# Kernel tuning notes

Measured on AMD Instinct MI355X. Metric: run time of the kernel, lower is better.

The kernel has to match this reference:

```python
import jax, jax.numpy as jnp
import numpy as np

B = 16; H = 64; WRES = 64; C = 512; NH = 16; WH = 8; WW = 8; PATCH = 4
N = WH * WW; HD = C // NH; R_MAX = PATCH * H; HID = 4 * C
PI = 3.141592653589793


def _rel_coords():
    yy, xx = np.meshgrid(np.arange(WH), np.arange(WW), indexing='ij')
    flat = np.stack([yy.ravel(), xx.ravel()])  # (2, N)
    rel = flat[:, :, None] - flat[:, None, :]  # (2, N, N)
    return rel[0].astype(np.int32), rel[1].astype(np.int32)

RAD_NP, AZ_NP = _rel_coords()


def _ln(x, g, b):
    m = x.mean(-1, keepdims=True)
    v = ((x - m) ** 2).mean(-1, keepdims=True)
    return (x - m) / jnp.sqrt(v + 1e-5) * g + b


def setup_inputs() -> dict:
    key = jax.random.key(0)
    ks = jax.random.split(key, 12)
    s = 0.02
    return {
        'x': jax.random.normal(ks[0], (B, H * WRES, C), jnp.float32),
        'D': jax.random.uniform(ks[1], (B, H, WRES), jnp.float32),
        'norm1_g': jnp.ones((C,), jnp.float32), 'norm1_b': jnp.zeros((C,), jnp.float32),
        'qkv_w': jax.random.normal(ks[2], (3 * C, C), jnp.float32) * s,
        'qkv_b': jnp.zeros((3 * C,), jnp.float32),
        'proj_w': jax.random.normal(ks[3], (C, C), jnp.float32) * s,
        'proj_b': jnp.zeros((C,), jnp.float32),
        'a_p': jax.random.normal(ks[4], (2 * WW - 1, NH), jnp.float32) * s,
        'b_p': jax.random.normal(ks[5], (2 * WW - 1, NH), jnp.float32) * s,
        'a_r': jax.random.normal(ks[6], (2 * WH - 1, NH), jnp.float32) * s,
        'b_r': jax.random.normal(ks[7], (2 * WH - 1, NH), jnp.float32) * s,
        'norm2_g': jnp.ones((C,), jnp.float32), 'norm2_b': jnp.zeros((C,), jnp.float32),
        'fc1_w': jax.random.normal(ks[8], (HID, C), jnp.float32) * s,
        'fc1_b': jnp.zeros((HID,), jnp.float32),
        'fc2_w': jax.random.normal(ks[9], (C, HID), jnp.float32) * s,
        'fc2_b': jnp.zeros((C,), jnp.float32),
    }


def reference(x, D, norm1_g, norm1_b, qkv_w, qkv_b, proj_w, proj_b,
              a_p, b_p, a_r, b_r, norm2_g, norm2_b, fc1_w, fc1_b, fc2_w, fc2_b):
    rad = jnp.asarray(RAD_NP)  # (N, N) relative row offsets in [-(WH-1), WH-1]
    az = jnp.asarray(AZ_NP)    # (N, N) relative col offsets
    shortcut = x
    xn = _ln(x, norm1_g, norm1_b).reshape(B, H, WRES, C)
    # window partition: (B,H,W,C) -> (nW*B, N, C); same for D -> (nW*B, N)
    xw = xn.reshape(B, H // WH, WH, WRES // WW, WW, C).transpose(0, 1, 3, 2, 4, 5).reshape(-1, N, C)
    Dw = D.reshape(B, H // WH, WH, WRES // WW, WW).transpose(0, 1, 3, 2, 4).reshape(-1, N)
    # qkv: (B_, N, 3C) -> q,k,v (B_, NH, N, HD)
    qkv = (xw @ qkv_w.T + qkv_b).reshape(-1, N, 3, NH, HD).transpose(2, 0, 3, 1, 4)
    q, k, v = qkv[0], qkv[1], qkv[2]
    q = q * (HD ** -0.5)
    attn = jnp.einsum('bhnd,bhmd->bhnm', q, k)
    # A_phi: gathered azimuth tables + trig, (N, N, NH). torch negative index == idx % size
    ip = az % (2 * WW - 1)
    azf = az.astype(jnp.float32) * (2.0 * PI / WRES)
    A_phi = a_p[ip] * jnp.cos(azf)[..., None] + b_p[ip] * jnp.sin(azf)[..., None]
    # A_r: per-window depth-modulated radius, (B_, N, N, NH); rad_final[b,i,j] = rad[i,j]*D[b,j]
    ir = rad % (2 * WH - 1)
    ang = (rad.astype(jnp.float32)[None] * Dw[:, None, :]) * (2.0 * PI / R_MAX)
    A_r = a_r[ir][None] * jnp.cos(ang)[..., None] + b_r[ir][None] * jnp.sin(ang)[..., None]
    attn = attn + jnp.transpose(A_phi, (2, 0, 1))[None] + jnp.transpose(A_r, (0, 3, 1, 2))
    attn = jax.nn.softmax(attn, axis=-1)
    out = jnp.einsum('bhnm,bhmd->bhnd', attn, v).transpose(0, 2, 1, 3).reshape(-1, N, C)
    out = out @ proj_w.T + proj_b
    # window reverse -> (B, H*W, C)
    xr = out.reshape(B, H // WH, WRES // WW, WH, WW, C).transpose(0, 1, 3, 2, 4, 5).reshape(B, H * WRES, C)
    x = shortcut + xr
    xm = _ln(x, norm2_g, norm2_b)
    h = jax.nn.gelu(xm @ fc1_w.T + fc1_b, approximate=False)
    return x + (h @ fc2_w.T + fc2_b)
```

## Files before the change

### kernel.cpp

```cpp
#include <hip/hip_runtime.h>
#include <hip/hip_bf16.h>
#include <math.h>

typedef __hip_bfloat16 bf16;
using f32x4  = __attribute__((ext_vector_type(4))) float;
using bf16x8 = __attribute__((ext_vector_type(8))) short;

static __device__ __forceinline__ float b2f(bf16 v) { return __bfloat162float(v); }
static __device__ __forceinline__ short f2b_s(float f) {
    bf16 b = __float2bfloat16(f);
    return *reinterpret_cast<short*>(&b);
}

static __device__ __forceinline__ void gl_lds16(const void* g, void* l) {
    __builtin_amdgcn_global_load_lds(
        (const __attribute__((address_space(1))) unsigned int*)g,
        (__attribute__((address_space(3))) unsigned int*)l, 16, 0, 0);
}

__global__ __launch_bounds__(256) void f2b_kernel(const float* __restrict__ in,
                                                  short* __restrict__ out, int n4)
{
    int i = blockIdx.x * 256 + threadIdx.x;
    if (i < n4) {
        float4 f = reinterpret_cast<const float4*>(in)[i];
        short4 s;
        s.x = f2b_s(f.x); s.y = f2b_s(f.y); s.z = f2b_s(f.z); s.w = f2b_s(f.w);
        reinterpret_cast<short4*>(out)[i] = s;
    }
}

__global__ __launch_bounds__(64) void ln_kernel(
    const float* __restrict__ in, const float* __restrict__ g,
    const float* __restrict__ bta, bf16* __restrict__ out, int windowed)
{
    int lr  = blockIdx.x;
    int tid = threadIdx.x;
    const float* xr = in + (size_t)lr * 512;
    int c0 = tid * 8;
    float4 f0 = *reinterpret_cast<const float4*>(xr + c0);
    float4 f1 = *reinterpret_cast<const float4*>(xr + c0 + 4);
    float v[8] = { f0.x, f0.y, f0.z, f0.w, f1.x, f1.y, f1.z, f1.w };
    float s = 0.f, s2 = 0.f;
#pragma unroll
    for (int k = 0; k < 8; ++k) { s += v[k]; s2 += v[k] * v[k]; }
#pragma unroll
    for (int off = 32; off; off >>= 1) {
        s  += __shfl_xor(s,  off, 64);
        s2 += __shfl_xor(s2, off, 64);
    }
    float mean = s * (1.0f / 512.0f);
    float var  = s2 * (1.0f / 512.0f) - mean * mean;
    float inv  = rsqrtf(var + 1e-5f);
    size_t drow;
    if (windowed) {
        int b_loc = lr >> 12;
        int l  = lr & 4095;
        int gr = l >> 6, gc = l & 63;
        int wy = gr >> 3, iy = gr & 7, wx = gc >> 3, ix = gc & 7;
        drow = (size_t)((b_loc * 64 + wy * 8 + wx) * 64 + iy * 8 + ix);
    } else {
        drow = (size_t)lr;
    }
    bf16* orow = out + drow * 512;
#pragma unroll
    for (int k = 0; k < 8; ++k) {
        int c = c0 + k;
        orow[c] = __float2bfloat16((v[k] - mean) * inv * g[c] + bta[c]);
    }
}

__global__ __launch_bounds__(256) void gemm_mfma(
    const bf16* __restrict__ A, const short* __restrict__ W,
    const float* __restrict__ bias, int N, int K, int mode,
    void* __restrict__ dstv, const float* __restrict__ res)
{
    __shared__ short As0[128 * 32];
    __shared__ short Bs0[128 * 32];
    __shared__ short As1[128 * 32];
    __shared__ short Bs1[128 * 32];

    int tid  = threadIdx.x;
    int wave = tid >> 6, lane = tid & 63;
    int waveM = wave >> 1, waveN = wave & 1;

    int nx  = gridDim.x;
    int nwg = nx * gridDim.y;
    int lid = blockIdx.y * nx + blockIdx.x;
    int nid = lid;
    if ((nwg & 7) == 0) nid = (lid & 7) * (nwg >> 3) + (lid >> 3);
    int mBase = (nid / nx) * 128;
    int nBase = (nid % nx) * 128;

    f32x4 acc[4][4] = {};

    int rr   = wave * 32 + (lane >> 2);
    int segE = (lane & 3) * 8;
    const bf16*  Ag = A + (size_t)(mBase + rr) * K + segE;
    const short* Bg = W + (size_t)(nBase + rr) * K + segE;
    size_t rs16 = (size_t)16 * K;

    int mf = waveM * 64 + (lane & 15);
    int nf = waveN * 64 + (lane & 15);
    int kq = (lane >> 4) * 8;

    auto stage = [&](int kb, short* Ad, short* Bd) {
        gl_lds16(Ag + kb,        Ad + wave * 1024);
        gl_lds16(Ag + kb + rs16, Ad + wave * 1024 + 512);
        gl_lds16(Bg + kb,        Bd + wave * 1024);
        gl_lds16(Bg + kb + rs16, Bd + wave * 1024 + 512);
    };
    auto compute = [&](const short* As_, const short* Bs_) {
        bf16x8 af[4], bfv[4];
#pragma unroll
        for (int i = 0; i < 4; ++i)
            af[i] = *reinterpret_cast<const bf16x8*>(&As_[(mf + i * 16) * 32 + kq]);
#pragma unroll
        for (int j = 0; j < 4; ++j)
            bfv[j] = *reinterpret_cast<const bf16x8*>(&Bs_[(nf + j * 16) * 32 + kq]);
#pragma unroll
        for (int i = 0; i < 4; ++i)
#pragma unroll
            for (int j = 0; j < 4; ++j)
                acc[i][j] = __builtin_amdgcn_mfma_f32_16x16x32_bf16(af[i], bfv[j], acc[i][j], 0, 0, 0);
    };

    stage(0, As0, Bs0);
    asm volatile("s_waitcnt vmcnt(0)" ::: "memory");
    __builtin_amdgcn_s_barrier();

    int nsteps = K >> 5;
    for (int t = 0; t < nsteps; t += 2) {
        stage((t + 1) << 5, As1, Bs1);
        compute(As0, Bs0);
        asm volatile("s_waitcnt vmcnt(0)" ::: "memory");
        __builtin_amdgcn_s_barrier();
        if (t + 2 < nsteps) stage((t + 2) << 5, As0, Bs0);
        compute(As1, Bs1);
        asm volatile("s_waitcnt vmcnt(0)" ::: "memory");
        __builtin_amdgcn_s_barrier();
    }

    int rq = (lane >> 4) * 4;
#pragma unroll
    for (int j = 0; j < 4; ++j) {
        int n = nBase + waveN * 64 + j * 16 + (lane & 15);
        float bn = bias[n];
#pragma unroll
        for (int i = 0; i < 4; ++i) {
#pragma unroll
            for (int reg = 0; reg < 4; ++reg) {
                int m = mBase + waveM * 64 + i * 16 + rq + reg;
                float v = acc[i][j][reg] + bn;
                if (mode == 0) {
                    ((bf16*)dstv)[(size_t)m * N + n] = __float2bfloat16(v);
                } else if (mode == 1) {
                    int b_loc = m >> 12, w = (m >> 6) & 63, tk = m & 63;
                    int wy = w >> 3, wx = w & 7, iy = tk >> 3, ix = tk & 7;
                    int l = ((wy << 3) + iy) * 64 + (wx << 3) + ix;
                    size_t idx = ((size_t)(b_loc * 4096 + l)) * 512 + n;
                    ((float*)dstv)[idx] = v + res[idx];
                } else if (mode == 2) {
                    float gl = 0.5f * v * (1.0f + erff(v * 0.70710678118654752f));
                    ((bf16*)dstv)[(size_t)m * N + n] = __float2bfloat16(gl);
                } else {
                    size_t idx = (size_t)m * N + n;
                    ((float*)dstv)[idx] = v + res[idx];
                }
            }
        }
    }
}

__global__ __launch_bounds__(256) void attn_kernel(
    const bf16* __restrict__ qkv, const float* __restrict__ Dofs,
    const float* __restrict__ a_p, const float* __restrict__ b_p,
    const float* __restrict__ a_r, const float* __restrict__ b_r,
    bf16* __restrict__ xattn)
{
    __shared__ float cosr[15][64];
    __shared__ float sinr[15][64];
    __shared__ float aphiS[15][16];
    __shared__ float arsS[15][16];
    __shared__ float brsS[15][16];
    __shared__ short Vt[32][72];
    __shared__ short Psh[64][72];

    int b_ = blockIdx.x;
    int bl = b_ >> 6;
    int w  = b_ & 63;
    int wy = w >> 3, wx = w & 7;
    int tid  = threadIdx.x;
    int wave = tid >> 6, lane = tid & 63;

    const float scale = 0.17677669529663687f;
    const float c_az  = 0.09817477042468103f;
    const float c_r   = 0.02454369260617026f;

    for (int t = tid; t < 960; t += 256) {
        int k = t >> 6;
        int j = t & 63;
        int jy = j >> 3, jx = j & 7;
        float Dj  = Dofs[(size_t)bl * 4096 + (wy * 8 + jy) * 64 + (wx * 8 + jx)];
        float ang = (float)(k - 7) * Dj * c_r;
        cosr[k][j] = __cosf(ang);
        sinr[k][j] = __sinf(ang);
    }
    if (tid < 240) {
        int k = tid >> 4;
        int h = tid & 15;
        int v = k - 7;
        int ip = v < 0 ? v + 15 : v;
        float azf = (float)v * c_az;
        aphiS[k][h] = a_p[ip * 16 + h] * __cosf(azf) + b_p[ip * 16 + h] * __sinf(azf);
        arsS[k][h]  = a_r[ip * 16 + h];
        brsS[k][h]  = b_r[ip * 16 + h];
    }

    int i_blk = wave;
    int l15 = lane & 15;
    int lq  = lane >> 4;
    int m0  = i_blk * 16 + lq * 4;
    const bf16* qbase = qkv + (size_t)(b_ * 64) * 1536;
    bf16* obase = xattn + (size_t)(b_ * 64) * 512;

    for (int h = 0; h < 16; ++h) {
        __syncthreads();
        {
            int tok = tid >> 2, dc = (tid & 3) * 8;
            bf16x8 vv = *reinterpret_cast<const bf16x8*>(
                qkv + (size_t)(b_ * 64 + tok) * 1536 + 1024 + h * 32 + dc);
#pragma unroll
            for (int s = 0; s < 8; ++s) Vt[dc + s][tok] = vv[s];
        }
        __syncthreads();

        bf16x8 af = *reinterpret_cast<const bf16x8*>(
            qbase + (size_t)(i_blk * 16 + l15) * 1536 + h * 32 + lq * 8);
        f32x4 Sacc[4] = {};
#pragma unroll
        for (int jb = 0; jb < 4; ++jb) {
            bf16x8 kf = *reinterpret_cast<const bf16x8*>(
                qbase + (size_t)(jb * 16 + l15) * 1536 + 512 + h * 32 + lq * 8);
            Sacc[jb] = __builtin_amdgcn_mfma_f32_16x16x32_bf16(af, kf, Sacc[jb], 0, 0, 0);
        }

        float Sv[4][4];
        float inv[4];
#pragma unroll
        for (int reg = 0; reg < 4; ++reg) {
            int m = m0 + reg;
            int iy = m >> 3, ix = m & 7;
            float rmax = -1e30f;
#pragma unroll
            for (int jb = 0; jb < 4; ++jb) {
                int n = jb * 16 + l15;
                int jy = n >> 3, jx = n & 7;
                int ai = ix - jx + 7;
                int ri = iy - jy + 7;
                float sc = Sacc[jb][reg] * scale + aphiS[ai][h]
                         + arsS[ri][h] * cosr[ri][n] + brsS[ri][h] * sinr[ri][n];
                Sv[reg][jb] = sc;
                rmax = fmaxf(rmax, sc);
            }
#pragma unroll
            for (int off = 1; off <= 8; off <<= 1)
                rmax = fmaxf(rmax, __shfl_xor(rmax, off, 64));
            float rsum = 0.f;
#pragma unroll
            for (int jb = 0; jb < 4; ++jb) {
                float e = __expf(Sv[reg][jb] - rmax);
                Sv[reg][jb] = e;
                rsum += e;
            }
#pragma unroll
            for (int off = 1; off <= 8; off <<= 1)
                rsum += __shfl_xor(rsum, off, 64);
            inv[reg] = 1.0f / rsum;
        }

#pragma unroll
        for (int reg = 0; reg < 4; ++reg)
#pragma unroll
            for (int jb = 0; jb < 4; ++jb)
                Psh[m0 + reg][jb * 16 + l15] = f2b_s(Sv[reg][jb]);

        f32x4 o[2] = {};
#pragma unroll
        for (int ks = 0; ks < 2; ++ks) {
            bf16x8 pa = *reinterpret_cast<const bf16x8*>(
                &Psh[i_blk * 16 + l15][ks * 32 + lq * 8]);
#pragma unroll
            for (int nb = 0; nb < 2; ++nb) {
                bf16x8 bv = *reinterpret_cast<const bf16x8*>(
                    &Vt[nb * 16 + l15][ks * 32 + lq * 8]);
                o[nb] = __builtin_amdgcn_mfma_f32_16x16x32_bf16(pa, bv, o[nb], 0, 0, 0);
            }
        }

#pragma unroll
        for (int nb = 0; nb < 2; ++nb) {
            int d = nb * 16 + l15;
#pragma unroll
            for (int reg = 0; reg < 4; ++reg) {
                int m = m0 + reg;
                obase[(size_t)m * 512 + h * 32 + d] = __float2bfloat16(o[nb][reg] * inv[reg]);
            }
        }
    }
}

extern "C" void kernel_launch(void* const* d_in, const int* in_sizes, int n_in,
                              void* d_out, int out_size, void* d_ws, size_t ws_size,
                              hipStream_t stream)
{
    const float* x      = (const float*)d_in[0];
    const float* D      = (const float*)d_in[1];
    const float* n1g    = (const float*)d_in[2];
    const float* n1b    = (const float*)d_in[3];
    const float* qkv_w  = (const float*)d_in[4];
    const float* qkv_b  = (const float*)d_in[5];
    const float* proj_w = (const float*)d_in[6];
    const float* proj_b = (const float*)d_in[7];
    const float* a_p    = (const float*)d_in[8];
    const float* b_p    = (const float*)d_in[9];
    const float* a_r    = (const float*)d_in[10];
    const float* b_r    = (const float*)d_in[11];
    const float* n2g    = (const float*)d_in[12];
    const float* n2b    = (const float*)d_in[13];
    const float* fc1_w  = (const float*)d_in[14];
    const float* fc1_b  = (const float*)d_in[15];
    const float* fc2_w  = (const float*)d_in[16];
    const float* fc2_b  = (const float*)d_in[17];
    float* out = (float*)d_out;

    char* ws = (char*)d_ws;
    short* qkv_wb  = (short*)ws;
    short* proj_wb = qkv_wb + 786432;
    short* fc1_wb  = proj_wb + 262144;
    short* fc2_wb  = fc1_wb + 1048576;
    char* gws = (char*)(fc2_wb + 1048576);

    int G = 16;
    while (G > 1 && 6291456 + (size_t)G * 4096 * 7168 > ws_size) G >>= 1;
    int NG = 16 / G;
    size_t rowsA = (size_t)G * 4096;

    float* x2   = (float*)gws;
    bf16*  xw   = (bf16*)(gws + rowsA * 2048);
    bf16*  qkvb = xw + rowsA * 512;
    bf16*  xatt = qkvb + rowsA * 1536;
    bf16*  xm   = xw;
    bf16*  hbuf = qkvb;

    hipLaunchKernelGGL(f2b_kernel, dim3(768),  dim3(256), 0, stream, qkv_w,  qkv_wb,  196608);
    hipLaunchKernelGGL(f2b_kernel, dim3(256),  dim3(256), 0, stream, proj_w, proj_wb,  65536);
    hipLaunchKernelGGL(f2b_kernel, dim3(1024), dim3(256), 0, stream, fc1_w,  fc1_wb,  262144);
    hipLaunchKernelGGL(f2b_kernel, dim3(1024), dim3(256), 0, stream, fc2_w,  fc2_wb,  262144);

    int gy = (int)(rowsA / 128);

    for (int g = 0; g < NG; ++g) {
        size_t r0 = (size_t)g * rowsA;
        hipLaunchKernelGGL(ln_kernel, dim3((int)rowsA), dim3(64), 0, stream,
                           x + r0 * 512, n1g, n1b, xw, 1);
        hipLaunchKernelGGL(gemm_mfma, dim3(1536 / 128, gy), dim3(256), 0, stream,
                           xw, qkv_wb, qkv_b, 1536, 512, 0, (void*)qkvb, (const float*)nullptr);
        hipLaunchKernelGGL(attn_kernel, dim3(G * 64), dim3(256), 0, stream,
                           qkvb, D + r0, a_p, b_p, a_r, b_r, xatt);
        hipLaunchKernelGGL(gemm_mfma, dim3(512 / 128, gy), dim3(256), 0, stream,
                           xatt, proj_wb, proj_b, 512, 512, 1, (void*)x2, x + r0 * 512);
        hipLaunchKernelGGL(ln_kernel, dim3((int)rowsA), dim3(64), 0, stream,
                           x2, n2g, n2b, xm, 0);
        hipLaunchKernelGGL(gemm_mfma, dim3(2048 / 128, gy), dim3(256), 0, stream,
                           xm, fc1_wb, fc1_b, 2048, 512, 2, (void*)hbuf, (const float*)nullptr);
        hipLaunchKernelGGL(gemm_mfma, dim3(512 / 128, gy), dim3(256), 0, stream,
                           hbuf, fc2_wb, fc2_b, 512, 2048, 3, (void*)(out + r0 * 512), x2);
    }
}
```

Before: 1.418 ms.

## Triple-buffer GEMM LDS staging with partial vmcnt waits

The GEMM's double-buffered K loop becomes a three-stage LDS ring that prefetches two K-tiles ahead. Each step waits with a partial s_waitcnt vmcnt instead of draining all loads, so global loads overlap more with MFMA compute. This adds 16 KB of LDS per block, which may reduce occupancy, and adds barriers and sched_barriers. The attention grid expression is rewritten but evaluates to the same value.

```diff
diff --git a/kernel.cpp b/kernel.cpp
--- a/kernel.cpp
+++ b/kernel.cpp
@@ -79,6 +79,8 @@
     __shared__ short Bs0[128 * 32];
     __shared__ short As1[128 * 32];
     __shared__ short Bs1[128 * 32];
+    __shared__ short As2[128 * 32];
+    __shared__ short Bs2[128 * 32];
 
     int tid  = threadIdx.x;
     int wave = tid >> 6, lane = tid & 63;
@@ -125,21 +127,33 @@
                 acc[i][j] = __builtin_amdgcn_mfma_f32_16x16x32_bf16(af[i], bfv[j], acc[i][j], 0, 0, 0);
     };
 
-    stage(0, As0, Bs0);
-    asm volatile("s_waitcnt vmcnt(0)" ::: "memory");
-    __builtin_amdgcn_s_barrier();
-
     int nsteps = K >> 5;
-    for (int t = 0; t < nsteps; t += 2) {
-        stage((t + 1) << 5, As1, Bs1);
-        compute(As0, Bs0);
-        asm volatile("s_waitcnt vmcnt(0)" ::: "memory");
-        __builtin_amdgcn_s_barrier();
-        if (t + 2 < nsteps) stage((t + 2) << 5, As0, Bs0);
-        compute(As1, Bs1);
-        asm volatile("s_waitcnt vmcnt(0)" ::: "memory");
-        __builtin_amdgcn_s_barrier();
-    }
+
+    stage(0,  As0, Bs0);
+    stage(32, As1, Bs1);
+
+#define SLOT(S, CA, CB, SA, SB)                                                  \
+    if ((S) < nsteps) {                                                          \
+        if ((S) + 2 < nsteps) stage(((S) + 2) << 5, SA, SB);                     \
+        if ((S) + 2 < nsteps)                                                    \
+            asm volatile("s_waitcnt vmcnt(8)" ::: "memory");                     \
+        else if ((S) + 1 < nsteps)                                               \
+            asm volatile("s_waitcnt vmcnt(4)" ::: "memory");                     \
+        else                                                                     \
+            asm volatile("s_waitcnt vmcnt(0)" ::: "memory");                     \
+        __builtin_amdgcn_s_barrier();                                            \
+        __builtin_amdgcn_sched_barrier(0);                                       \
+        compute(CA, CB);                                                         \
+        __builtin_amdgcn_sched_barrier(0);                                       \
+        __builtin_amdgcn_s_barrier();                                            \
+    }
+
+    for (int s = 0; s < nsteps; s += 3) {
+        SLOT(s,     As0, Bs0, As2, Bs2);
+        SLOT(s + 1, As1, Bs1, As0, Bs0);
+        SLOT(s + 2, As2, Bs2, As1, Bs1);
+    }
+#undef SLOT
 
     int rq = (lane >> 4) * 4;
 #pragma unroll
@@ -366,7 +380,7 @@
                            x + r0 * 512, n1g, n1b, xw, 1);
         hipLaunchKernelGGL(gemm_mfma, dim3(1536 / 128, gy), dim3(256), 0, stream,
                            xw, qkv_wb, qkv_b, 1536, 512, 0, (void*)qkvb, (const float*)nullptr);
-        hipLaunchKernelGGL(attn_kernel, dim3(G * 64), dim3(256), 0, stream,
+        hipLaunchKernelGGL(attn_kernel, dim3(G * 1024 / 16), dim3(256), 0, stream,
                            qkvb, D + r0, a_p, b_p, a_r, b_r, xatt);
         hipLaunchKernelGGL(gemm_mfma, dim3(512 / 128, gy), dim3(256), 0, stream,
                            xatt, proj_wb, proj_b, 512, 512, 1, (void*)x2, x + r0 * 512);
```

Measured after the change: 1.374 ms. 3.1% less time.
